# Kernel tuning notes

Measured on AMD Instinct MI355X. Metric: run time of the kernel, lower is better.

The kernel has to match this reference:

```python
import jax, jax.numpy as jnp
import numpy as np

K = 3
PAD = 1


def _deform_conv(x, offset, weight, bias):
    """torchvision-style deform_conv2d (v1, no mask), stride=1, pad=1, dil=1.
    x: [B,C,H,W], offset: [B,2*K*K,H,W] ordered (dy,dx) per kernel pos (row-major).
    """
    B, C, H, W = x.shape
    K2 = K * K
    off = offset.reshape(B, K2, 2, H, W)
    dy, dx = off[:, :, 0], off[:, :, 1]
    ky = jnp.repeat(jnp.arange(K), K).astype(x.dtype)  # [K2] kernel row offsets
    kx = jnp.tile(jnp.arange(K), K).astype(x.dtype)    # [K2] kernel col offsets
    hh = jnp.arange(H, dtype=x.dtype)
    ww = jnp.arange(W, dtype=x.dtype)
    # sampling positions: [B,K2,H,W]
    py = hh[None, None, :, None] + ky[None, :, None, None] - PAD + dy
    px = ww[None, None, None, :] + kx[None, :, None, None] - PAD + dx
    y0f = jnp.floor(py)
    x0f = jnp.floor(px)
    wy = py - y0f
    wx = px - x0f
    y0 = y0f.astype(jnp.int32)
    x0 = x0f.astype(jnp.int32)
    xf = x.reshape(B, C, H * W)

    def corner(iy, ix, w):
        # zero padding outside the image: contribution masked to 0
        valid = (iy >= 0) & (iy < H) & (ix >= 0) & (ix < W)
        iyc = jnp.clip(iy, 0, H - 1)
        ixc = jnp.clip(ix, 0, W - 1)
        lin = (iyc * W + ixc).reshape(B, -1)                      # [B,K2*H*W]
        g = jnp.take_along_axis(xf, lin[:, None, :], axis=2)     # [B,C,K2*H*W]
        g = g.reshape(B, C, K2, H, W)
        wv = (w * valid.astype(x.dtype))[:, None]                # [B,1,K2,H,W]
        return g * wv

    val = (corner(y0, x0, (1 - wy) * (1 - wx))
           + corner(y0, x0 + 1, (1 - wy) * wx)
           + corner(y0 + 1, x0, wy * (1 - wx))
           + corner(y0 + 1, x0 + 1, wy * wx))                    # [B,C,K2,H,W]
    O = weight.shape[0]
    out = jnp.einsum('ock,bckhw->bohw', weight.reshape(O, C, K2), val)
    return out + bias[None, :, None, None]


def setup_inputs() -> dict:
    key = jax.random.key(0)
    k1, k2, k3, k4, k5 = jax.random.split(key, 5)
    B, C, O, H, W = 4, 64, 64, 128, 128
    fan = C * K * K
    x = jax.random.normal(k1, (B, C, H, W), dtype=jnp.float32)
    w_off = jax.random.normal(k2, (2 * K * K, C, K, K), dtype=jnp.float32) / np.sqrt(fan)
    b_off = jax.random.normal(k3, (2 * K * K,), dtype=jnp.float32) * 0.01
    w_dcn = jax.random.normal(k4, (O, C, K, K), dtype=jnp.float32) / np.sqrt(fan)
    b_dcn = jax.random.normal(k5, (O,), dtype=jnp.float32) * 0.01
    return {"x": x, "w_off": w_off, "b_off": b_off, "w_dcn": w_dcn, "b_dcn": b_dcn}


def reference(x, w_off, b_off, w_dcn, b_dcn):
    offset = jax.lax.conv_general_dilated(
        x, w_off, window_strides=(1, 1), padding=((PAD, PAD), (PAD, PAD)),
        dimension_numbers=('NCHW', 'OIHW', 'NCHW')) + b_off[None, :, None, None]
    return _deform_conv(x, offset, w_dcn, b_dcn)
```

## Files before the change

kernel.cpp:

```cpp
#include <hip/hip_runtime.h>
#include <hip/hip_fp16.h>

#define HH 128
#define WW 128
#define CC 64
#define OO 64
#define HWSZ (HH*WW)

typedef _Float16 f16x8 __attribute__((ext_vector_type(8)));
typedef float    f32x4 __attribute__((ext_vector_type(4)));

__device__ __forceinline__ unsigned short f2h(float f) {
    return __half_as_ushort(__float2half_rn(f));
}

__global__ __launch_bounds__(256) void prep_all(const float* __restrict__ x,
                                                const float* __restrict__ wd,
                                                const float* __restrict__ wo,
                                                unsigned short* __restrict__ xh,
                                                unsigned short* __restrict__ wdtf,
                                                unsigned short* __restrict__ wotf) {
    int t = threadIdx.x;
    if (blockIdx.z == 4) {
        int i = (blockIdx.y * 2 + blockIdx.x) * 256 + t;
        if (i < 36864) {
            int j = i & 7, l = (i >> 3) & 63, nt = (i >> 9) & 3, kcb = i >> 11;
            int k = kcb >> 1, cb = kcb & 1;
            int o = nt * 16 + (l & 15);
            int c = cb * 32 + ((l >> 4) & 3) * 8 + j;
            wdtf[i] = f2h(wd[(o * 64 + c) * 9 + k]);
        } else if (i < 36864 + 18432) {
            int jdx = i - 36864;
            int j = jdx & 7, l = (jdx >> 3) & 63, nt = (jdx >> 9) & 1, kcb = jdx >> 10;
            int k = kcb >> 1, cb = kcb & 1;
            int oc = nt * 16 + (l & 15);
            int c = cb * 32 + ((l >> 4) & 3) * 8 + j;
            wotf[jdx] = f2h(oc < 18 ? wo[(oc * 64 + c) * 9 + k] : 0.0f);
        }
        return;
    }
    __shared__ float tile[64 * 65];
    int w0 = blockIdx.x * 64, h = blockIdx.y, b = blockIdx.z;
    const float* xb = x + ((long)b * CC * HWSZ) + h * WW + w0;
#pragma unroll
    for (int i = 0; i < 16; ++i) {
        int idx = i * 256 + t; int c = idx >> 6, w = idx & 63;
        tile[c * 65 + w] = xb[c * HWSZ + w];
    }
    __syncthreads();
    unsigned short* xo = xh + ((long)((b * HH + h) * WW + w0)) * CC;
#pragma unroll
    for (int i = 0; i < 8; ++i) {
        int idx = i * 256 + t; int w = idx >> 5, c = (idx & 31) * 2;
        ushort2 u;
        u.x = f2h(tile[c * 65 + w]);
        u.y = f2h(tile[(c + 1) * 65 + w]);
        *(ushort2*)(xo + w * CC + c) = u;
    }
}

__global__ __launch_bounds__(256, 3) void fused_dcn(const unsigned short* __restrict__ xh,
                                                    const unsigned short* __restrict__ wotf,
                                                    const float* __restrict__ b_off,
                                                    const unsigned short* __restrict__ wdtf,
                                                    const float* __restrict__ b_dcn,
                                                    float* __restrict__ out) {
    __shared__ __attribute__((aligned(16))) unsigned short shm[32 * 584];
    __shared__ float offs[64 * 20];
    unsigned short* xr    = shm;
    unsigned short* val_s = shm;

    int id = blockIdx.x;
    int c8 = id & 7;
    int j  = id >> 3;
    int g  = (j >> 5) * 8 + c8;
    int inner = j & 31;
    int b  = g >> 3;
    int h  = (g & 7) * 16 + (inner >> 1);
    int w0 = (inner & 1) * 64;

    int t = threadIdx.x;
    int l = t & 63, wv = t >> 6;
    int m = l & 15, q = l >> 4;

#pragma unroll
    for (int i = 0; i < 7; ++i) {
        int idx = i * 256 + t;
        if (idx < 1584) {
            int r = idx / 528;
            int rem = idx - r * 528;
            int p = rem >> 3, cc = rem & 7;
            int y = h + r - 1, wx = w0 - 1 + p;
            uint4 v = make_uint4(0u, 0u, 0u, 0u);
            if (((unsigned)y < HH) && ((unsigned)wx < WW))
                v = *(const uint4*)(xh + ((long)((b * HH + y) * WW + wx)) * CC + cc * 8);
            *(uint4*)&xr[(r * 68 + p) * 72 + cc * 8] = v;
        }
    }
    __syncthreads();
    {
        int px0 = wv * 16;
        f32x4 acc0 = {0.f, 0.f, 0.f, 0.f}, acc1 = {0.f, 0.f, 0.f, 0.f};
#pragma unroll
        for (int k = 0; k < 9; ++k) {
            int ky = k / 3, kx = k - ky * 3;
            const unsigned short* ar = &xr[(ky * 68 + px0 + m + kx) * 72 + q * 8];
            f16x8 a0 = *(const f16x8*)(ar);
            f16x8 a1 = *(const f16x8*)(ar + 32);
            const unsigned short* bk = wotf + (k * 2) * 2 * 512 + l * 8;
            f16x8 b00 = *(const f16x8*)(bk);
            f16x8 b01 = *(const f16x8*)(bk + 512);
            f16x8 b10 = *(const f16x8*)(bk + 1024);
            f16x8 b11 = *(const f16x8*)(bk + 1536);
            acc0 = __builtin_amdgcn_mfma_f32_16x16x32_f16(a0, b00, acc0, 0, 0, 0);
            acc0 = __builtin_amdgcn_mfma_f32_16x16x32_f16(a1, b10, acc0, 0, 0, 0);
            acc1 = __builtin_amdgcn_mfma_f32_16x16x32_f16(a0, b01, acc1, 0, 0, 0);
            acc1 = __builtin_amdgcn_mfma_f32_16x16x32_f16(a1, b11, acc1, 0, 0, 0);
        }
        float bo0 = b_off[m];
#pragma unroll
        for (int r = 0; r < 4; ++r)
            offs[(px0 + q * 4 + r) * 20 + m] = acc0[r] + bo0;
        if (m < 2) {
            float bo1 = b_off[16 + m];
#pragma unroll
            for (int r = 0; r < 4; ++r)
                offs[(px0 + q * 4 + r) * 20 + 16 + m] = acc1[r] + bo1;
        }
    }
    __syncthreads();

    int spx = t >> 3, ch8 = (t & 7) * 8;

    f16x8 Breg[18];
#pragma unroll
    for (int kc = 0; kc < 18; ++kc)
        Breg[kc] = *(const f16x8*)(wdtf + (kc * 4 + wv) * 512 + l * 8);

    const unsigned short* xb = xh + (long)b * HWSZ * CC;
    int o = wv * 16 + m;
    float bo = b_dcn[o];
    float* outo = out + ((long)(b * OO + o)) * HWSZ + h * WW;

#pragma unroll
    for (int g2 = 0; g2 < 2; ++g2) {
        int wg0 = w0 + g2 * 32;
        const float* oprow = &offs[(g2 * 32 + spx) * 20];

#pragma unroll
        for (int k = 0; k < 9; ++k) {
            int ky = k / 3, kx = k - ky * 3;
            float2 ov = *(const float2*)(oprow + 2 * k);
            float py  = (float)(h + ky - 1) + ov.x;
            float pxf = (float)(wg0 + spx + kx - 1) + ov.y;
            float y0f = floorf(py), x0f = floorf(pxf);
            float wy = py - y0f, wx = pxf - x0f;
            int y0 = (int)y0f, x0 = (int)x0f, y1 = y0 + 1, x1 = x0 + 1;
            bool vy0 = (unsigned)y0 < HH, vy1 = (unsigned)y1 < HH;
            bool vx0 = (unsigned)x0 < WW, vx1 = (unsigned)x1 < WW;
            int y0c = min(max(y0, 0), HH - 1), y1c = min(max(y1, 0), HH - 1);
            int x0c = min(max(x0, 0), WW - 1), x1c = min(max(x1, 0), WW - 1);
            _Float16 h0w = (_Float16)((vy0 && vx0) ? (1.f - wy) * (1.f - wx) : 0.f);
            _Float16 h1w = (_Float16)((vy0 && vx1) ? (1.f - wy) * wx : 0.f);
            _Float16 h2w = (_Float16)((vy1 && vx0) ? wy * (1.f - wx) : 0.f);
            _Float16 h3w = (_Float16)((vy1 && vx1) ? wy * wx : 0.f);
            f16x8 s00 = *(const f16x8*)(xb + (y0c * WW + x0c) * CC + ch8);
            f16x8 s01 = *(const f16x8*)(xb + (y0c * WW + x1c) * CC + ch8);
            f16x8 s10 = *(const f16x8*)(xb + (y1c * WW + x0c) * CC + ch8);
            f16x8 s11 = *(const f16x8*)(xb + (y1c * WW + x1c) * CC + ch8);
            f16x8 a = s00 * h0w + s01 * h1w + s10 * h2w + s11 * h3w;
            *(f16x8*)&val_s[spx * 584 + k * 64 + ch8] = a;
        }
        __syncthreads();

        f32x4 acc0 = {0.f, 0.f, 0.f, 0.f}, acc1 = {0.f, 0.f, 0.f, 0.f};
#pragma unroll
        for (int kc = 0; kc < 18; ++kc) {
            f16x8 a0 = *(const f16x8*)&val_s[m * 584 + kc * 32 + q * 8];
            f16x8 a1 = *(const f16x8*)&val_s[(16 + m) * 584 + kc * 32 + q * 8];
            acc0 = __builtin_amdgcn_mfma_f32_16x16x32_f16(a0, Breg[kc], acc0, 0, 0, 0);
            acc1 = __builtin_amdgcn_mfma_f32_16x16x32_f16(a1, Breg[kc], acc1, 0, 0, 0);
        }

        f32x4 r0 = acc0, r1 = acc1;
        r0[0] += bo; r0[1] += bo; r0[2] += bo; r0[3] += bo;
        r1[0] += bo; r1[1] += bo; r1[2] += bo; r1[3] += bo;
        *(f32x4*)(outo + wg0 + q * 4) = r0;
        *(f32x4*)(outo + wg0 + 16 + q * 4) = r1;
        if (g2 == 0) __syncthreads();
    }
}

extern "C" void kernel_launch(void* const* d_in, const int* in_sizes, int n_in,
                              void* d_out, int out_size, void* d_ws, size_t ws_size,
                              hipStream_t stream) {
    const float* x     = (const float*)d_in[0];
    const float* w_off = (const float*)d_in[1];
    const float* b_off = (const float*)d_in[2];
    const float* w_dcn = (const float*)d_in[3];
    const float* b_dcn = (const float*)d_in[4];
    float* out = (float*)d_out;

    char* ws = (char*)d_ws;
    unsigned short* xh   = (unsigned short*)ws;
    unsigned short* wdtf = (unsigned short*)(ws + 8388608);
    unsigned short* wotf = (unsigned short*)(ws + 8462336);

    hipLaunchKernelGGL(prep_all, dim3(2, 128, 5), dim3(256), 0, stream,
                       x, w_dcn, w_off, xh, wdtf, wotf);
    hipLaunchKernelGGL(fused_dcn, dim3(1024), dim3(256), 0, stream,
                       xh, wotf, b_off, wdtf, b_dcn, out);
}
```

Baseline: 101.5 us.

## Split deform sampling into two tap segments to cut LDS and registers

Splits the 9-tap bilinear sampling and MFMA accumulation into two segments (5 and 4 taps), so the staging buffer in shared memory shrinks. Removes the 18-register weight cache and streams weights from global memory per MFMA step. Raises launch bounds to 4 blocks per CU and adds s_setprio around the MFMA phases. Trades extra barriers and repeated weight loads for higher occupancy to hide gather latency.

```diff
diff --git a/kernel.cpp b/kernel.cpp
--- a/kernel.cpp
+++ b/kernel.cpp
@@ -59,14 +59,70 @@
     }
 }
 
-__global__ __launch_bounds__(256, 3) void fused_dcn(const unsigned short* __restrict__ xh,
+#define VST 328
+#define OST 18
+
+template<int K0, int KN>
+__device__ __forceinline__ void sample_seg(const unsigned short* __restrict__ xb,
+                                           const float* __restrict__ oprow,
+                                           unsigned short* __restrict__ val_s,
+                                           int h, int wpx, int spx, int ch8) {
+#pragma unroll
+    for (int k = K0; k < K0 + KN; ++k) {
+        int ky = k / 3, kx = k - ky * 3;
+        float2 ov = *(const float2*)(oprow + 2 * k);
+        float py  = (float)(h + ky - 1) + ov.x;
+        float pxf = (float)(wpx + kx - 1) + ov.y;
+        float y0f = floorf(py), x0f = floorf(pxf);
+        float wy = py - y0f, wx = pxf - x0f;
+        int y0 = (int)y0f, x0 = (int)x0f, y1 = y0 + 1, x1 = x0 + 1;
+        bool vy0 = (unsigned)y0 < HH, vy1 = (unsigned)y1 < HH;
+        bool vx0 = (unsigned)x0 < WW, vx1 = (unsigned)x1 < WW;
+        int y0c = min(max(y0, 0), HH - 1), y1c = min(max(y1, 0), HH - 1);
+        int x0c = min(max(x0, 0), WW - 1), x1c = min(max(x1, 0), WW - 1);
+        _Float16 h0w = (_Float16)((vy0 && vx0) ? (1.f - wy) * (1.f - wx) : 0.f);
+        _Float16 h1w = (_Float16)((vy0 && vx1) ? (1.f - wy) * wx : 0.f);
+        _Float16 h2w = (_Float16)((vy1 && vx0) ? wy * (1.f - wx) : 0.f);
+        _Float16 h3w = (_Float16)((vy1 && vx1) ? wy * wx : 0.f);
+        f16x8 s00 = *(const f16x8*)(xb + (y0c * WW + x0c) * CC + ch8);
+        f16x8 s01 = *(const f16x8*)(xb + (y0c * WW + x1c) * CC + ch8);
+        f16x8 s10 = *(const f16x8*)(xb + (y1c * WW + x0c) * CC + ch8);
+        f16x8 s11 = *(const f16x8*)(xb + (y1c * WW + x1c) * CC + ch8);
+        f16x8 a = s00 * h0w + s01 * h1w + s10 * h2w + s11 * h3w;
+        *(f16x8*)&val_s[spx * VST + (k - K0) * 64 + ch8] = a;
+    }
+}
+
+template<int K0, int KN>
+__device__ __forceinline__ void mfma_seg(const unsigned short* __restrict__ val_s,
+                                         const unsigned short* __restrict__ wdtf,
+                                         int m, int q, int wv, int l,
+                                         f32x4& acc0, f32x4& acc1) {
+#pragma unroll
+    for (int ki = 0; ki < KN; ++ki) {
+        const unsigned short* vs = &val_s[m * VST + ki * 64 + q * 8];
+        f16x8 a00 = *(const f16x8*)(vs);
+        f16x8 a01 = *(const f16x8*)(vs + 32);
+        f16x8 a10 = *(const f16x8*)(vs + 16 * VST);
+        f16x8 a11 = *(const f16x8*)(vs + 16 * VST + 32);
+        int kcg = (K0 + ki) * 2;
+        f16x8 b0 = *(const f16x8*)(wdtf + (kcg * 4 + wv) * 512 + l * 8);
+        f16x8 b1 = *(const f16x8*)(wdtf + ((kcg + 1) * 4 + wv) * 512 + l * 8);
+        acc0 = __builtin_amdgcn_mfma_f32_16x16x32_f16(a00, b0, acc0, 0, 0, 0);
+        acc1 = __builtin_amdgcn_mfma_f32_16x16x32_f16(a10, b0, acc1, 0, 0, 0);
+        acc0 = __builtin_amdgcn_mfma_f32_16x16x32_f16(a01, b1, acc0, 0, 0, 0);
+        acc1 = __builtin_amdgcn_mfma_f32_16x16x32_f16(a11, b1, acc1, 0, 0, 0);
+    }
+}
+
+__global__ __launch_bounds__(256, 4) void fused_dcn(const unsigned short* __restrict__ xh,
                                                     const unsigned short* __restrict__ wotf,
                                                     const float* __restrict__ b_off,
                                                     const unsigned short* __restrict__ wdtf,
                                                     const float* __restrict__ b_dcn,
                                                     float* __restrict__ out) {
-    __shared__ __attribute__((aligned(16))) unsigned short shm[32 * 584];
-    __shared__ float offs[64 * 20];
+    __shared__ __attribute__((aligned(16))) unsigned short shm[3 * 68 * 72];
+    __shared__ __attribute__((aligned(16))) float offs[64 * OST];
     unsigned short* xr    = shm;
     unsigned short* val_s = shm;
 
@@ -120,22 +176,17 @@
         float bo0 = b_off[m];
 #pragma unroll
         for (int r = 0; r < 4; ++r)
-            offs[(px0 + q * 4 + r) * 20 + m] = acc0[r] + bo0;
+            offs[(px0 + q * 4 + r) * OST + m] = acc0[r] + bo0;
         if (m < 2) {
             float bo1 = b_off[16 + m];
 #pragma unroll
             for (int r = 0; r < 4; ++r)
-                offs[(px0 + q * 4 + r) * 20 + 16 + m] = acc1[r] + bo1;
+                offs[(px0 + q * 4 + r) * OST + 16 + m] = acc1[r] + bo1;
         }
     }
     __syncthreads();
 
     int spx = t >> 3, ch8 = (t & 7) * 8;
-
-    f16x8 Breg[18];
-#pragma unroll
-    for (int kc = 0; kc < 18; ++kc)
-        Breg[kc] = *(const f16x8*)(wdtf + (kc * 4 + wv) * 512 + l * 8);
 
     const unsigned short* xb = xh + (long)b * HWSZ * CC;
     int o = wv * 16 + m;
@@ -145,42 +196,23 @@
 #pragma unroll
     for (int g2 = 0; g2 < 2; ++g2) {
         int wg0 = w0 + g2 * 32;
-        const float* oprow = &offs[(g2 * 32 + spx) * 20];
-
-#pragma unroll
-        for (int k = 0; k < 9; ++k) {
-            int ky = k / 3, kx = k - ky * 3;
-            float2 ov = *(const float2*)(oprow + 2 * k);
-            float py  = (float)(h + ky - 1) + ov.x;
-            float pxf = (float)(wg0 + spx + kx - 1) + ov.y;
-            float y0f = floorf(py), x0f = floorf(pxf);
-            float wy = py - y0f, wx = pxf - x0f;
-            int y0 = (int)y0f, x0 = (int)x0f, y1 = y0 + 1, x1 = x0 + 1;
-            bool vy0 = (unsigned)y0 < HH, vy1 = (unsigned)y1 < HH;
-            bool vx0 = (unsigned)x0 < WW, vx1 = (unsigned)x1 < WW;
-            int y0c = min(max(y0, 0), HH - 1), y1c = min(max(y1, 0), HH - 1);
-            int x0c = min(max(x0, 0), WW - 1), x1c = min(max(x1, 0), WW - 1);
-            _Float16 h0w = (_Float16)((vy0 && vx0) ? (1.f - wy) * (1.f - wx) : 0.f);
-            _Float16 h1w = (_Float16)((vy0 && vx1) ? (1.f - wy) * wx : 0.f);
-            _Float16 h2w = (_Float16)((vy1 && vx0) ? wy * (1.f - wx) : 0.f);
-            _Float16 h3w = (_Float16)((vy1 && vx1) ? wy * wx : 0.f);
-            f16x8 s00 = *(const f16x8*)(xb + (y0c * WW + x0c) * CC + ch8);
-            f16x8 s01 = *(const f16x8*)(xb + (y0c * WW + x1c) * CC + ch8);
-            f16x8 s10 = *(const f16x8*)(xb + (y1c * WW + x0c) * CC + ch8);
-            f16x8 s11 = *(const f16x8*)(xb + (y1c * WW + x1c) * CC + ch8);
-            f16x8 a = s00 * h0w + s01 * h1w + s10 * h2w + s11 * h3w;
-            *(f16x8*)&val_s[spx * 584 + k * 64 + ch8] = a;
-        }
+        const float* oprow = &offs[(g2 * 32 + spx) * OST];
+        int wpx = wg0 + spx;
+
+        f32x4 acc0 = {0.f, 0.f, 0.f, 0.f}, acc1 = {0.f, 0.f, 0.f, 0.f};
+
+        sample_seg<0, 5>(xb, oprow, val_s, h, wpx, spx, ch8);
         __syncthreads();
-
-        f32x4 acc0 = {0.f, 0.f, 0.f, 0.f}, acc1 = {0.f, 0.f, 0.f, 0.f};
-#pragma unroll
-        for (int kc = 0; kc < 18; ++kc) {
-            f16x8 a0 = *(const f16x8*)&val_s[m * 584 + kc * 32 + q * 8];
-            f16x8 a1 = *(const f16x8*)&val_s[(16 + m) * 584 + kc * 32 + q * 8];
-            acc0 = __builtin_amdgcn_mfma_f32_16x16x32_f16(a0, Breg[kc], acc0, 0, 0, 0);
-            acc1 = __builtin_amdgcn_mfma_f32_16x16x32_f16(a1, Breg[kc], acc1, 0, 0, 0);
-        }
+        __builtin_amdgcn_s_setprio(1);
+        mfma_seg<0, 5>(val_s, wdtf, m, q, wv, l, acc0, acc1);
+        __builtin_amdgcn_s_setprio(0);
+        __syncthreads();
+
+        sample_seg<5, 4>(xb, oprow, val_s, h, wpx, spx, ch8);
+        __syncthreads();
+        __builtin_amdgcn_s_setprio(1);
+        mfma_seg<5, 4>(val_s, wdtf, m, q, wv, l, acc0, acc1);
+        __builtin_amdgcn_s_setprio(0);
 
         f32x4 r0 = acc0, r1 = acc1;
         r0[0] += bo; r0[1] += bo; r0[2] += bo; r0[3] += bo;
```

After: 101.3 us. No clear change (-0.2%).
